# Performance work log

Hardware: AMD Instinct MI355X
Metric: run time of the kernel (lower is better)

## Reference

```python
import jax, jax.numpy as jnp
import numpy as np

NG = 1024      # graphs
NPG = 128      # nodes per graph (forced by lin1 = Linear(128*hid, 128))
N = NG * NPG   # 131072 nodes
DEG = 16       # avg in-graph degree
E = N * DEG    # 2,097,152 edges
IN, H = 4, 64


def setup_inputs() -> dict:
    key = jax.random.key(0)
    ks = jax.random.split(key, 24)
    x = jax.random.normal(ks[0], (N, IN), jnp.float32)
    # edges constrained within each 128-node graph
    src = jax.random.randint(ks[1], (E,), 0, NPG)
    dst = jax.random.randint(ks[2], (E,), 0, NPG)
    off = jnp.repeat(jnp.arange(NG, dtype=jnp.int32) * NPG, NPG * DEG)
    edge_index = jnp.stack([src.astype(jnp.int32) + off, dst.astype(jnp.int32) + off])
    g = lambda k, shp, fan: jax.random.normal(k, shp, jnp.float32) / np.float32(np.sqrt(fan))
    return {
        "x": x, "edge_index": edge_index,
        # GATv2Conv(4->64)
        "Wl": g(ks[3], (IN, H), IN), "bl": jnp.zeros((H,), jnp.float32),
        "Wr": g(ks[4], (IN, H), IN), "br": jnp.zeros((H,), jnp.float32),
        "att_v2": g(ks[5], (H,), H), "b_v2": jnp.zeros((H,), jnp.float32),
        # GATConv #1 (64->64)
        "Wg1": g(ks[6], (H, H), H), "as1": g(ks[7], (H,), H),
        "ad1": g(ks[8], (H,), H), "bg1": jnp.zeros((H,), jnp.float32),
        # GATConv #2 (64->64)
        "Wg2": g(ks[9], (H, H), H), "as2": g(ks[10], (H,), H),
        "ad2": g(ks[11], (H,), H), "bg2": jnp.zeros((H,), jnp.float32),
        # LayerNorm(64)
        "ln_g": jnp.ones((H,), jnp.float32), "ln_b": jnp.zeros((H,), jnp.float32),
        # heads: Linear(128*64 -> 128), Linear(128 -> 1)
        "W1": g(ks[12], (NPG * H, 128), NPG * H), "b1": jnp.zeros((128,), jnp.float32),
        "W2": g(ks[13], (128, 1), 128), "b2": jnp.zeros((1,), jnp.float32),
    }


def _seg_softmax(logits, seg):
    # stable softmax over edges grouped by destination node
    m = jax.ops.segment_max(logits, seg, num_segments=N)
    ex = jnp.exp(logits - m[seg])
    s = jax.ops.segment_sum(ex, seg, num_segments=N)
    return ex / (s[seg] + 1e-16)


def _gatv2(x, src, dst, Wl, bl, Wr, br, att, bias):
    xl = x @ Wl + bl                       # source transform [N,H]
    xr = x @ Wr + br                       # target transform [N,H]
    e = jax.nn.leaky_relu(xl[src] + xr[dst], 0.2) @ att   # [E]
    a = _seg_softmax(e, dst)
    out = jax.ops.segment_sum(a[:, None] * xl[src], dst, num_segments=N)
    return out + bias


def _gat(x, src, dst, W, a_src, a_dst, bias):
    # GATConv default: add self-loops
    loop = jnp.arange(N, dtype=src.dtype)
    s2 = jnp.concatenate([src, loop]); d2 = jnp.concatenate([dst, loop])
    xw = x @ W                             # [N,H]
    al_s = xw @ a_src; al_d = xw @ a_dst   # per-node attention halves [N]
    e = jax.nn.leaky_relu(al_s[s2] + al_d[d2], 0.2)
    a = _seg_softmax(e, d2)
    out = jax.ops.segment_sum(a[:, None] * xw[s2], d2, num_segments=N)
    return out + bias


def _layernorm(x, g, b, eps=1e-5):
    mu = jnp.mean(x, -1, keepdims=True)
    var = jnp.mean(jnp.square(x - mu), -1, keepdims=True)
    return (x - mu) * jax.lax.rsqrt(var + eps) * g + b


def reference(x, edge_index, Wl, bl, Wr, br, att_v2, b_v2,
              Wg1, as1, ad1, bg1, Wg2, as2, ad2, bg2,
              ln_g, ln_b, W1, b1, W2, b2):
    src, dst = edge_index[0], edge_index[1]
    h = jax.nn.leaky_relu(_gatv2(x, src, dst, Wl, bl, Wr, br, att_v2, b_v2), 0.01)
    h = _layernorm(h, ln_g, ln_b)
    h = jax.nn.relu(_gat(h, src, dst, Wg1, as1, ad1, bg1))
    h = jax.nn.relu(_gat(h, src, dst, Wg2, as2, ad2, bg2))
    # linearize: batch is sorted with exactly NPG nodes per graph -> reshape
    h = h.reshape(NG, NPG * H)
    h = jax.nn.leaky_relu(h @ W1 + b1, 0.01)
    return jax.nn.sigmoid(h @ W2 + b2)     # [NG, 1]
```

## Files before the change

### kernel.cpp

```cpp
#include <hip/hip_runtime.h>
#include <hip/hip_bf16.h>

#define NGRAPH 1024
#define NPG 128
#define NTOT (NGRAPH*NPG)
#define EPG 2048
#define ETOT (NTOT*16)
#define HD 64

typedef unsigned int uint;
typedef unsigned short ushort_t;
typedef __attribute__((ext_vector_type(8))) short s8v;
typedef __attribute__((ext_vector_type(4))) float f32x4;

#define MFMA16 __builtin_amdgcn_mfma_f32_16x16x32_bf16

__device__ __forceinline__ float lrelu(float x, float s){ return fmaxf(x, x*s); }
__device__ __forceinline__ float b2lo(uint u){ return __uint_as_float(u << 16); }
__device__ __forceinline__ float b2hi(uint u){ return __uint_as_float(u & 0xFFFF0000u); }
__device__ __forceinline__ uint pkbf(float a, float b){
  union { __hip_bfloat162 h; uint u; } t;
  t.h = __hip_bfloat162{__float2bfloat16(a), __float2bfloat16(b)};
  return t.u;
}
__device__ __forceinline__ ushort_t bfb(float v){
  __hip_bfloat16 h = __float2bfloat16(v);
  union { __hip_bfloat16 h; ushort_t u; } t; t.h = h; return t.u;
}
union U4S8 { uint4 u; s8v s; };
__device__ __forceinline__ s8v bcs8(uint4 u){ U4S8 t; t.u = u; return t.s; }
__device__ __forceinline__ s8v pk8(uint4 x, uint4 y){
  U4S8 t;
  t.u.x = pkbf(__uint_as_float(x.x), __uint_as_float(x.y));
  t.u.y = pkbf(__uint_as_float(x.z), __uint_as_float(x.w));
  t.u.z = pkbf(__uint_as_float(y.x), __uint_as_float(y.y));
  t.u.w = pkbf(__uint_as_float(y.z), __uint_as_float(y.w));
  return t.s;
}

#define DPP_ADD(v, ctrl) ((v) + __int_as_float(__builtin_amdgcn_update_dpp(0, __float_as_int(v), (ctrl), 0xF, 0xF, false)))

__device__ __forceinline__ int oswz(int r, int p){ return (r<<5) | ((((p>>2) ^ (r & 7))<<2) | (p & 3)); }
__device__ __forceinline__ int obase(int r, int oc){ return (r<<5) | (((oc) ^ (r & 7))<<2); }
__device__ __forceinline__ int t64(int r, int p){ return (r<<6) | ((((p>>2) ^ (r & 15))<<2) | (p & 3)); }
__device__ __forceinline__ int t64b(int r, int q){ return (r<<6) | (((q ^ (r & 15))<<2)); }
__device__ __forceinline__ int fP(int r, int k){ return (r<<7) | (((((k>>2) ^ r) & 31)<<2) | (k & 3)); }
__device__ __forceinline__ int fPb(int r, int q){ return (r<<7) | ((((q ^ r) & 31))<<2); }

#define O_A   0
#define O_B   4096
#define O_P   8192
#define O_E   12288
#define O_ED  14336
#define O_SOF 15360
#define O_SPO 15489
#define O_NMV 15617
#define O_SSE 15745
#define O_ALS 15873
#define O_ALD 16001
#define O_WAS 16132
#define O_WAD 16196
#define SM_SZ 16260

__global__ __launch_bounds__(256) void gnn_fused(
    const float* __restrict__ x, const int* __restrict__ ei,
    const float* __restrict__ Wl, const float* __restrict__ bl,
    const float* __restrict__ Wr, const float* __restrict__ br,
    const float* __restrict__ att, const float* __restrict__ bv2,
    const float* __restrict__ Wg1, const float* __restrict__ as1,
    const float* __restrict__ ad1, const float* __restrict__ bg1,
    const float* __restrict__ Wg2, const float* __restrict__ as2,
    const float* __restrict__ ad2, const float* __restrict__ bg2,
    const float* __restrict__ lng, const float* __restrict__ lnb,
    uint* __restrict__ hout)
{
  __shared__ uint SM[SM_SZ];
  uint*     sXl  = SM + O_A;
  uint*     sXr  = SM + O_B;
  float*    Pf   = (float*)(SM + O_P);
  float*    eva  = (float*)(SM + O_E);
  ushort_t* edsd = (ushort_t*)(SM + O_ED);
  int*      soff = (int*)(SM + O_SOF);
  int*      spos = (int*)(SM + O_SPO);
  float*    nmv  = (float*)(SM + O_NMV);
  float*    sse  = (float*)(SM + O_SSE);
  float*    als  = (float*)(SM + O_ALS);
  float*    ald  = (float*)(SM + O_ALD);
  float*    was  = (float*)(SM + O_WAS);
  float*    wad  = (float*)(SM + O_WAD);
  ushort_t* sH16 = (ushort_t*)(SM + O_A);
  ushort_t* sT16 = (ushort_t*)(SM + O_B);
  ushort_t* wg16 = (ushort_t*)(SM + O_E);

  const int g    = blockIdx.x;
  const int tid  = threadIdx.x;
  const int lane = tid & 63;
  const int wv   = tid >> 6;
  const int lw   = lane & 15;
  const int lq   = lane >> 4;
  const int oc   = lane & 7;
  const int ebase = g * EPG;

  if (tid < NPG) spos[tid] = 0;
  __syncthreads();
  for (int e = tid; e < EPG; e += 256)
    atomicAdd(&spos[ei[ETOT + ebase + e] - g*NPG], 1);
  __syncthreads();
  if (wv == 0) {
    int c0 = spos[lane], c1 = spos[lane + 64];
    #pragma unroll
    for (int o = 1; o < 64; o <<= 1) { int t = __shfl_up(c0, o); if (lane >= o) c0 += t; }
    #pragma unroll
    for (int o = 1; o < 64; o <<= 1) { int t = __shfl_up(c1, o); if (lane >= o) c1 += t; }
    int tot0 = __shfl(c0, 63);
    soff[lane + 1]  = c0;
    soff[lane + 65] = c1 + tot0;
    if (lane == 0) soff[0] = 0;
  }
  __syncthreads();
  if (tid < NPG) spos[tid] = soff[tid];
  __syncthreads();
  for (int e = tid; e < EPG; e += 256) {
    int s = ei[ebase + e] - g*NPG;
    int d = ei[ETOT + ebase + e] - g*NPG;
    int p = atomicAdd(&spos[d], 1);
    edsd[p] = (ushort_t)(s | (d << 8));
  }

  {
    const int pl = lane & 31, hb = lane >> 5;
    const float2 wl0 = *(const float2*)&Wl[0*64 + 2*pl];
    const float2 wl1 = *(const float2*)&Wl[1*64 + 2*pl];
    const float2 wl2 = *(const float2*)&Wl[2*64 + 2*pl];
    const float2 wl3 = *(const float2*)&Wl[3*64 + 2*pl];
    const float2 wr0 = *(const float2*)&Wr[0*64 + 2*pl];
    const float2 wr1 = *(const float2*)&Wr[1*64 + 2*pl];
    const float2 wr2 = *(const float2*)&Wr[2*64 + 2*pl];
    const float2 wr3 = *(const float2*)&Wr[3*64 + 2*pl];
    const float2 blp = *(const float2*)&bl[2*pl];
    const float2 brp = *(const float2*)&br[2*pl];
    const float4* x4 = (const float4*)x + (size_t)g * NPG;
    __syncthreads();
    for (int st = 0; st < 16; st++) {
      int i = st*8 + wv*2 + hb;
      float4 xi = x4[i];
      float l0 = blp.x + xi.x*wl0.x + xi.y*wl1.x + xi.z*wl2.x + xi.w*wl3.x;
      float l1 = blp.y + xi.x*wl0.y + xi.y*wl1.y + xi.z*wl2.y + xi.w*wl3.y;
      float r0 = brp.x + xi.x*wr0.x + xi.y*wr1.x + xi.z*wr2.x + xi.w*wr3.x;
      float r1 = brp.y + xi.x*wr0.y + xi.y*wr1.y + xi.z*wr2.y + xi.w*wr3.y;
      sXl[oswz(i, pl)] = pkbf(l0, l1);
      sXr[oswz(i, pl)] = pkbf(r0, r1);
    }
  }
  __syncthreads();

  {
    const int grp = lane >> 3;
    float4 atA = *(const float4*)&att[oc*8];
    float4 atB = *(const float4*)&att[oc*8 + 4];
    int base = wv * 512;
    for (int stp = 0; stp < 64; stp++) {
      int e  = base + stp*8 + grp;
      int sd = edsd[e];
      int s  = sd & 127, d = sd >> 8;
      uint4 ql = *(uint4*)&sXl[obase(s, oc)];
      uint4 qr = *(uint4*)&sXr[obase(d, oc)];
      float acc, v;
      v = b2lo(ql.x)+b2lo(qr.x); acc  = lrelu(v,0.2f)*atA.x;
      v = b2hi(ql.x)+b2hi(qr.x); acc += lrelu(v,0.2f)*atA.y;
      v = b2lo(ql.y)+b2lo(qr.y); acc += lrelu(v,0.2f)*atA.z;
      v = b2hi(ql.y)+b2hi(qr.y); acc += lrelu(v,0.2f)*atA.w;
      v = b2lo(ql.z)+b2lo(qr.z); acc += lrelu(v,0.2f)*atB.x;
      v = b2hi(ql.z)+b2hi(qr.z); acc += lrelu(v,0.2f)*atB.y;
      v = b2lo(ql.w)+b2lo(qr.w); acc += lrelu(v,0.2f)*atB.z;
      v = b2hi(ql.w)+b2hi(qr.w); acc += lrelu(v,0.2f)*atB.w;
      acc = DPP_ADD(acc, 0x111); acc = DPP_ADD(acc, 0x112); acc = DPP_ADD(acc, 0x114);
      if ((lane & 7) == 7) eva[e] = acc;
    }
  }
  __syncthreads();

  {
    const int g16 = tid >> 4, sl = tid & 15;
    for (int it = 0; it < 8; it++) {
      int d = it*16 + g16;
      int p0 = soff[d], p1 = soff[d+1];
      float m = -1e30f;
      for (int p = p0 + sl; p < p1; p += 16) m = fmaxf(m, eva[p]);
      #pragma unroll
      for (int o = 1; o < 16; o <<= 1) m = fmaxf(m, __shfl_xor(m, o));
      float ssum = 0.f;
      for (int p = p0 + sl; p < p1; p += 16) {
        float ex = __expf(eva[p] - m); ssum += ex; eva[p] = ex;
      }
      #pragma unroll
      for (int o = 1; o < 16; o <<= 1) ssum += __shfl_xor(ssum, o);
      if (sl == 0) nmv[d] = 1.f / (ssum + 1e-16f);
    }
    ushort_t* xl16 = (ushort_t*)(SM + O_A);
    int j = tid & 63, spb = tid >> 6;
    for (int i = 0; i < 16; i++) {
      int sp = spb*16 + i;
      float v0 = __uint_as_float((uint)xl16[oswz(2*sp,   j>>1)*2 + (j&1)] << 16);
      float v1 = __uint_as_float((uint)xl16[oswz(2*sp+1, j>>1)*2 + (j&1)] << 16);
      sXr[t64(j, sp)] = pkbf(v0, v1);
    }
  }
  __syncthreads();

  {
    int n0 = 32*(wv>>1), m0 = 16*(wv&1);
    float bja = bv2[n0 + lw], bjb = bv2[n0 + 16 + lw];
    for (int q = 0; q < 4; q++) {
      #pragma unroll
      for (int i = 0; i < 4; i++) { uint4 z = {0,0,0,0}; *(uint4*)&SM[O_P + (tid + i*256)*4] = z; }
      __syncthreads();
      int p0 = soff[q*32], p1 = soff[q*32 + 32];
      for (int p = p0 + tid; p < p1; p += 256) {
        int sd = edsd[p]; int s = sd & 127, d = sd >> 8;
        atomicAdd(&Pf[fP(d - q*32, s)], eva[p] * nmv[d]);
      }
      __syncthreads();
      f32x4 c0 = {0.f,0.f,0.f,0.f}, c1 = {0.f,0.f,0.f,0.f};
      int row = m0 + lw;
      #pragma unroll
      for (int ks = 0; ks < 4; ks++) {
        int kk = ks*32 + lq*8;
        uint4 f0 = *(uint4*)&Pf[fPb(row, kk>>2)];
        uint4 f1 = *(uint4*)&Pf[fPb(row, (kk>>2)+1)];
        s8v a = pk8(f0, f1);
        s8v b0 = bcs8(*(uint4*)&SM[O_B + t64b(n0 + lw,      kk>>3)]);
        s8v b1 = bcs8(*(uint4*)&SM[O_B + t64b(n0 + 16 + lw, kk>>3)]);
        c0 = MFMA16(a, b0, c0, 0, 0, 0);
        c1 = MFMA16(a, b1, c1, 0, 0, 0);
      }
      int rg0 = q*32 + m0 + lq*4;
      #pragma unroll
      for (int rg = 0; rg < 4; rg++) {
        float v0 = lrelu(c0[rg] + bja, 0.01f);
        float v1 = lrelu(c1[rg] + bjb, 0.01f);
        int jc0 = n0 + lw, jc1 = n0 + 16 + lw;
        sH16[oswz(rg0+rg, jc0>>1)*2 + (jc0&1)] = bfb(v0);
        sH16[oswz(rg0+rg, jc1>>1)*2 + (jc1&1)] = bfb(v1);
      }
      __syncthreads();
    }
  }

  {
    int pl = lane & 31, hb = lane >> 5;
    float2 gv = *(const float2*)&lng[2*pl];
    float2 bv = *(const float2*)&lnb[2*pl];
    for (int it = 0; it < 16; it++) {
      int d = it*8 + wv*2 + hb;
      uint w = SM[O_A + oswz(d, pl)];
      float v0 = b2lo(w), v1 = b2hi(w);
      float s1 = v0 + v1, s2 = v0*v0 + v1*v1;
      #pragma unroll
      for (int o = 1; o < 32; o <<= 1) { s1 += __shfl_xor(s1, o); s2 += __shfl_xor(s2, o); }
      float mu  = s1 * 0.015625f;
      float var = s2 * 0.015625f - mu*mu;
      float rs  = rsqrtf(var + 1e-5f);
      v0 = (v0 - mu)*rs*gv.x + bv.x;
      v1 = (v1 - mu)*rs*gv.y + bv.y;
      SM[O_A + oswz(d, pl)] = pkbf(v0, v1);
    }
  }
  __syncthreads();

  for (int layer = 0; layer < 2; layer++) {
    const float* Wg  = layer ? Wg2 : Wg1;
    const float* avs = layer ? as2 : as1;
    const float* avd = layer ? ad2 : ad1;
    const float* bg  = layer ? bg2 : bg1;

    if (tid < 128) {
      const float* av = (tid < 64) ? avs : avd;
      float* dst = (tid < 64) ? was : wad;
      int k = tid & 63;
      float acc = 0.f;
      #pragma unroll
      for (int jj = 0; jj < 16; jj++) {
        float4 w = *(const float4*)&Wg[k*64 + jj*4];
        float4 a = *(const float4*)&av[jj*4];
        acc += w.x*a.x + w.y*a.y + w.z*a.z + w.w*a.w;
      }
      dst[k] = acc;
    } else {
      int t2 = tid - 128;
      #pragma unroll
      for (int i = 0; i < 8; i++) {
        int idx = t2 + i*128;
        int k = idx >> 4, j4 = (idx & 15)*4;
        float4 w = *(const float4*)&Wg[k*64 + j4];
        wg16[oswz(j4+0, k>>1)*2 + (k&1)] = bfb(w.x);
        wg16[oswz(j4+1, k>>1)*2 + (k&1)] = bfb(w.y);
        wg16[oswz(j4+2, k>>1)*2 + (k&1)] = bfb(w.z);
        wg16[oswz(j4+3, k>>1)*2 + (k&1)] = bfb(w.w);
      }
    }
    __syncthreads();

    {
      int row = 16*wv + lw;
      s8v a0 = bcs8(*(uint4*)&SM[O_E + obase(row, lq)]);
      s8v a1 = bcs8(*(uint4*)&SM[O_E + obase(row, 4+lq)]);
      #pragma unroll
      for (int nt = 0; nt < 8; nt++) {
        int d = nt*16 + lw;
        s8v b0 = bcs8(*(uint4*)&SM[O_A + obase(d, lq)]);
        s8v b1 = bcs8(*(uint4*)&SM[O_A + obase(d, 4+lq)]);
        f32x4 c = {0.f,0.f,0.f,0.f};
        c = MFMA16(a0, b0, c, 0, 0, 0);
        c = MFMA16(a1, b1, c, 0, 0, 0);
        int j0 = 16*wv + lq*4;
        #pragma unroll
        for (int rg = 0; rg < 4; rg++)
          sT16[t64(j0+rg, d>>1)*2 + (d&1)] = bfb(c[rg]);
      }
    }
    __syncthreads();

    {
      float4 ws0 = *(float4*)&was[oc*8], ws1 = *(float4*)&was[oc*8 + 4];
      float4 wd0 = *(float4*)&wad[oc*8], wd1 = *(float4*)&wad[oc*8 + 4];
      for (int ps = 0; ps < 4; ps++) {
        int n = ps*32 + (tid >> 3);
        uint4 q = *(uint4*)&SM[O_A + obase(n, oc)];
        float f0=b2lo(q.x), f1=b2hi(q.x), f2=b2lo(q.y), f3=b2hi(q.y);
        float f4=b2lo(q.z), f5=b2hi(q.z), f6=b2lo(q.w), f7=b2hi(q.w);
        float sa = f0*ws0.x+f1*ws0.y+f2*ws0.z+f3*ws0.w+f4*ws1.x+f5*ws1.y+f6*ws1.z+f7*ws1.w;
        float sd = f0*wd0.x+f1*wd0.y+f2*wd0.z+f3*wd0.w+f4*wd1.x+f5*wd1.y+f6*wd1.z+f7*wd1.w;
        sa = DPP_ADD(sa, 0x111); sa = DPP_ADD(sa, 0x112); sa = DPP_ADD(sa, 0x114);
        sd = DPP_ADD(sd, 0x111); sd = DPP_ADD(sd, 0x112); sd = DPP_ADD(sd, 0x114);
        if ((lane & 7) == 7) { als[n] = sa; ald[n] = sd; }
      }
    }
    __syncthreads();

    #pragma unroll
    for (int i = 0; i < 8; i++) {
      int e = tid + i*256;
      int sd = edsd[e];
      eva[e] = lrelu(als[sd & 127] + ald[sd >> 8], 0.2f);
    }
    __syncthreads();

    {
      const int g16 = tid >> 4, sl = tid & 15;
      for (int it = 0; it < 8; it++) {
        int d = it*16 + g16;
        int p0 = soff[d], p1 = soff[d+1];
        float se = lrelu(als[d] + ald[d], 0.2f);
        float m = se;
        for (int p = p0 + sl; p < p1; p += 16) m = fmaxf(m, eva[p]);
        #pragma unroll
        for (int o = 1; o < 16; o <<= 1) m = fmaxf(m, __shfl_xor(m, o));
        float ex0 = __expf(se - m);
        float ssum = 0.f;
        for (int p = p0 + sl; p < p1; p += 16) {
          float ex = __expf(eva[p] - m); ssum += ex; eva[p] = ex;
        }
        #pragma unroll
        for (int o = 1; o < 16; o <<= 1) ssum += __shfl_xor(ssum, o);
        if (sl == 0) { nmv[d] = 1.f / (ssum + ex0 + 1e-16f); sse[d] = ex0; }
      }
    }
    __syncthreads();

    {
      int n0 = 32*(wv>>1), m0 = 16*(wv&1);
      float bja = bg[n0 + lw], bjb = bg[n0 + 16 + lw];
      for (int q = 0; q < 4; q++) {
        #pragma unroll
        for (int i = 0; i < 4; i++) { uint4 z = {0,0,0,0}; *(uint4*)&SM[O_P + (tid + i*256)*4] = z; }
        __syncthreads();
        int p0 = soff[q*32], p1 = soff[q*32 + 32];
        for (int p = p0 + tid; p < p1; p += 256) {
          int sd = edsd[p]; int s = sd & 127, d = sd >> 8;
          atomicAdd(&Pf[fP(d - q*32, s)], eva[p] * nmv[d]);
        }
        if (tid < 32) { int d = q*32 + tid; atomicAdd(&Pf[fP(tid, d)], sse[d] * nmv[d]); }
        __syncthreads();
        f32x4 c0 = {0.f,0.f,0.f,0.f}, c1 = {0.f,0.f,0.f,0.f};
        int row = m0 + lw;
        #pragma unroll
        for (int ks = 0; ks < 4; ks++) {
          int kk = ks*32 + lq*8;
          uint4 f0 = *(uint4*)&Pf[fPb(row, kk>>2)];
          uint4 f1 = *(uint4*)&Pf[fPb(row, (kk>>2)+1)];
          s8v a = pk8(f0, f1);
          s8v b0 = bcs8(*(uint4*)&SM[O_B + t64b(n0 + lw,      kk>>3)]);
          s8v b1 = bcs8(*(uint4*)&SM[O_B + t64b(n0 + 16 + lw, kk>>3)]);
          c0 = MFMA16(a, b0, c0, 0, 0, 0);
          c1 = MFMA16(a, b1, c1, 0, 0, 0);
        }
        int rg0 = q*32 + m0 + lq*4;
        #pragma unroll
        for (int rg = 0; rg < 4; rg++) {
          float v0 = fmaxf(c0[rg] + bja, 0.f);
          float v1 = fmaxf(c1[rg] + bjb, 0.f);
          int jc0 = n0 + lw, jc1 = n0 + 16 + lw;
          sH16[oswz(rg0+rg, jc0>>1)*2 + (jc0&1)] = bfb(v0);
          sH16[oswz(rg0+rg, jc1>>1)*2 + (jc1&1)] = bfb(v1);
        }
        __syncthreads();
      }
    }
  }

  {
    uint* hg = hout + (size_t)g * 4096;
    #pragma unroll
    for (int i = 0; i < 16; i++) {
      int idx = tid + i*256;
      hg[idx] = SM[O_A + oswz(idx >> 5, idx & 31)];
    }
  }
}

__global__ __launch_bounds__(256) void w1_transpose(const float* __restrict__ W1,
                                                    uint* __restrict__ w1t)
{
  __shared__ float sw[64*130];
  const int tid = threadIdx.x;
  const int k0 = blockIdx.x * 64;
  #pragma unroll
  for (int i = 0; i < 8; i++) {
    int idx = tid + i*256;
    int r = idx >> 5, c4 = (idx & 31)*4;
    *(float4*)&sw[r*130 + c4] = *(const float4*)&W1[(size_t)(k0+r)*128 + c4];
  }
  __syncthreads();
  #pragma unroll
  for (int i = 0; i < 16; i++) {
    int idx = tid + i*256;
    int c = idx >> 5, kp = idx & 31;
    w1t[(size_t)c*4096 + (k0>>1) + kp] = pkbf(sw[(2*kp)*130 + c], sw[(2*kp+1)*130 + c]);
  }
}

__global__ __launch_bounds__(256) void head_gemm(
    const uint* __restrict__ hbuf, const uint* __restrict__ w1t,
    float* __restrict__ partial)
{
  __shared__ uint sAh[2048];
  __shared__ uint sBh[4096];
  const int tid = threadIdx.x, lane = tid & 63, wv = tid >> 6;
  const int lw = lane & 15, lq = lane >> 4;
  const int g0 = blockIdx.x * 64;
  const int ks = blockIdx.y;
  f32x4 acc[8];
  #pragma unroll
  for (int i = 0; i < 8; i++) acc[i] = f32x4{0.f,0.f,0.f,0.f};

  for (int ch = 0; ch < 8; ch++) {
    int pb = ks*256 + ch*32;
    #pragma unroll
    for (int i = 0; i < 2; i++) {
      int idx = tid + i*256; int r = idx >> 3, q4 = idx & 7;
      uint4 v = *(const uint4*)&hbuf[(size_t)(g0+r)*4096 + pb + q4*4];
      *(uint4*)&sAh[(r<<5) | ((q4 ^ (r & 7))<<2)] = v;
    }
    #pragma unroll
    for (int i = 0; i < 4; i++) {
      int idx = tid + i*256; int r = idx >> 3, q4 = idx & 7;
      uint4 v = *(const uint4*)&w1t[(size_t)r*4096 + pb + q4*4];
      *(uint4*)&sBh[(r<<5) | ((q4 ^ (r & 7))<<2)] = v;
    }
    __syncthreads();
    int ra = 16*wv + lw;
    s8v a0 = bcs8(*(uint4*)&sAh[obase(ra, lq)]);
    s8v a1 = bcs8(*(uint4*)&sAh[obase(ra, 4+lq)]);
    #pragma unroll
    for (int nt = 0; nt < 8; nt++) {
      int c = nt*16 + lw;
      s8v b0 = bcs8(*(uint4*)&sBh[obase(c, lq)]);
      s8v b1 = bcs8(*(uint4*)&sBh[obase(c, 4+lq)]);
      acc[nt] = MFMA16(a0, b0, acc[nt], 0, 0, 0);
      acc[nt] = MFMA16(a1, b1, acc[nt], 0, 0, 0);
    }
    __syncthreads();
  }
  float* pp = partial + (size_t)ks*131072;
  #pragma unroll
  for (int nt = 0; nt < 8; nt++) {
    int c = nt*16 + lw;
    int r0 = g0 + 16*wv + lq*4;
    #pragma unroll
    for (int rg = 0; rg < 4; rg++)
      pp[(size_t)(r0+rg)*128 + c] = acc[nt][rg];
  }
}

__global__ __launch_bounds__(64) void head_out(
    const float* __restrict__ partial, const float* __restrict__ b1,
    const float* __restrict__ W2, const float* __restrict__ b2,
    float* __restrict__ out)
{
  const int g = blockIdx.x;
  const int l = threadIdx.x;
  float v0 = b1[l], v1 = b1[64 + l];
  #pragma unroll
  for (int s = 0; s < 16; s++) {
    v0 += partial[(size_t)s*131072 + g*128 + l];
    v1 += partial[(size_t)s*131072 + g*128 + 64 + l];
  }
  float sum = lrelu(v0, 0.01f)*W2[l] + lrelu(v1, 0.01f)*W2[64 + l];
  #pragma unroll
  for (int m = 32; m > 0; m >>= 1) sum += __shfl_xor(sum, m);
  if (l == 0) out[g] = 1.f / (1.f + __expf(-(sum + b2[0])));
}

extern "C" void kernel_launch(void* const* d_in, const int* in_sizes, int n_in,
                              void* d_out, int out_size, void* d_ws, size_t ws_size,
                              hipStream_t stream) {
  const float* x   = (const float*)d_in[0];
  const int*   ei  = (const int*)  d_in[1];
  const float* Wl  = (const float*)d_in[2];
  const float* bl_ = (const float*)d_in[3];
  const float* Wr  = (const float*)d_in[4];
  const float* br_ = (const float*)d_in[5];
  const float* att = (const float*)d_in[6];
  const float* bv2 = (const float*)d_in[7];
  const float* Wg1 = (const float*)d_in[8];
  const float* as1 = (const float*)d_in[9];
  const float* ad1 = (const float*)d_in[10];
  const float* bg1 = (const float*)d_in[11];
  const float* Wg2 = (const float*)d_in[12];
  const float* as2 = (const float*)d_in[13];
  const float* ad2 = (const float*)d_in[14];
  const float* bg2 = (const float*)d_in[15];
  const float* lng = (const float*)d_in[16];
  const float* lnb = (const float*)d_in[17];
  const float* W1  = (const float*)d_in[18];
  const float* b1  = (const float*)d_in[19];
  const float* W2  = (const float*)d_in[20];
  const float* b2  = (const float*)d_in[21];
  float* out = (float*)d_out;

  uint*  hbuf    = (uint*)d_ws;
  float* partial = (float*)((char*)d_ws + (size_t)16*1024*1024);
  uint*  w1t     = (uint*)((char*)d_ws + (size_t)24*1024*1024);

  w1_transpose<<<128, 256, 0, stream>>>(W1, w1t);
  gnn_fused<<<NGRAPH, 256, 0, stream>>>(x, ei, Wl, bl_, Wr, br_, att, bv2,
      Wg1, as1, ad1, bg1, Wg2, as2, ad2, bg2, lng, lnb, hbuf);
  head_gemm<<<dim3(16, 16), 256, 0, stream>>>(hbuf, w1t, partial);
  head_out<<<NGRAPH, 64, 0, stream>>>(partial, b1, W2, b2, out);
}
```

Measured before the change: 287.5 us.

## Shrink shared memory: fp16 edge weights, smaller aggregation tiles, recompute GAT logits

Edge attention values are now stored as fp16 in a half-size buffer, and raw GATv2 logits reuse the P scratch region. The dense aggregation works on 16 destination rows per pass instead of 32, so the P tile is halved. The GAT logit pass is dropped and logits are recomputed inside the softmax loops. Together these cut LDS per block from about 65KB to 53KB, aiming for more resident blocks per CU. The cost is twice as many aggregation passes and barriers, and a small precision loss from fp16 edge weights.

```diff
diff --git a/kernel.cpp b/kernel.cpp
--- a/kernel.cpp
+++ b/kernel.cpp
@@ -50,17 +50,17 @@
 #define O_A   0
 #define O_B   4096
 #define O_P   8192
-#define O_E   12288
-#define O_ED  14336
-#define O_SOF 15360
-#define O_SPO 15489
-#define O_NMV 15617
-#define O_SSE 15745
-#define O_ALS 15873
-#define O_ALD 16001
-#define O_WAS 16132
-#define O_WAD 16196
-#define SM_SZ 16260
+#define O_EV  10240
+#define O_ED  11264
+#define O_SOF 12288
+#define O_SPO 12417
+#define O_NMV 12545
+#define O_SSE 12673
+#define O_ALS 12801
+#define O_ALD 12929
+#define O_WAS 13060
+#define O_WAD 13124
+#define SM_SZ 13188
 
 __global__ __launch_bounds__(256) void gnn_fused(
     const float* __restrict__ x, const int* __restrict__ ei,
@@ -75,22 +75,22 @@
     uint* __restrict__ hout)
 {
   __shared__ uint SM[SM_SZ];
-  uint*     sXl  = SM + O_A;
-  uint*     sXr  = SM + O_B;
-  float*    Pf   = (float*)(SM + O_P);
-  float*    eva  = (float*)(SM + O_E);
-  ushort_t* edsd = (ushort_t*)(SM + O_ED);
-  int*      soff = (int*)(SM + O_SOF);
-  int*      spos = (int*)(SM + O_SPO);
-  float*    nmv  = (float*)(SM + O_NMV);
-  float*    sse  = (float*)(SM + O_SSE);
-  float*    als  = (float*)(SM + O_ALS);
-  float*    ald  = (float*)(SM + O_ALD);
-  float*    was  = (float*)(SM + O_WAS);
-  float*    wad  = (float*)(SM + O_WAD);
-  ushort_t* sH16 = (ushort_t*)(SM + O_A);
-  ushort_t* sT16 = (ushort_t*)(SM + O_B);
-  ushort_t* wg16 = (ushort_t*)(SM + O_E);
+  uint*      sXl  = SM + O_A;
+  uint*      sXr  = SM + O_B;
+  float*     Pf   = (float*)(SM + O_P);
+  _Float16*  evh  = (_Float16*)(SM + O_EV);
+  ushort_t*  edsd = (ushort_t*)(SM + O_ED);
+  int*       soff = (int*)(SM + O_SOF);
+  int*       spos = (int*)(SM + O_SPO);
+  float*     nmv  = (float*)(SM + O_NMV);
+  float*     sse  = (float*)(SM + O_SSE);
+  float*     als  = (float*)(SM + O_ALS);
+  float*     ald  = (float*)(SM + O_ALD);
+  float*     was  = (float*)(SM + O_WAS);
+  float*     wad  = (float*)(SM + O_WAD);
+  ushort_t*  sH16 = (ushort_t*)(SM + O_A);
+  ushort_t*  sT16 = (ushort_t*)(SM + O_B);
+  ushort_t*  wg16 = (ushort_t*)(SM + O_P);
 
   const int g    = blockIdx.x;
   const int tid  = threadIdx.x;
@@ -175,7 +175,7 @@
       v = b2lo(ql.w)+b2lo(qr.w); acc += lrelu(v,0.2f)*atB.z;
       v = b2hi(ql.w)+b2hi(qr.w); acc += lrelu(v,0.2f)*atB.w;
       acc = DPP_ADD(acc, 0x111); acc = DPP_ADD(acc, 0x112); acc = DPP_ADD(acc, 0x114);
-      if ((lane & 7) == 7) eva[e] = acc;
+      if ((lane & 7) == 7) Pf[e] = acc;
     }
   }
   __syncthreads();
@@ -186,12 +186,12 @@
       int d = it*16 + g16;
       int p0 = soff[d], p1 = soff[d+1];
       float m = -1e30f;
-      for (int p = p0 + sl; p < p1; p += 16) m = fmaxf(m, eva[p]);
+      for (int p = p0 + sl; p < p1; p += 16) m = fmaxf(m, Pf[p]);
       #pragma unroll
       for (int o = 1; o < 16; o <<= 1) m = fmaxf(m, __shfl_xor(m, o));
       float ssum = 0.f;
       for (int p = p0 + sl; p < p1; p += 16) {
-        float ex = __expf(eva[p] - m); ssum += ex; eva[p] = ex;
+        float ex = __expf(Pf[p] - m); ssum += ex; evh[p] = (_Float16)ex;
       }
       #pragma unroll
       for (int o = 1; o < 16; o <<= 1) ssum += __shfl_xor(ssum, o);
@@ -209,39 +209,34 @@
   __syncthreads();
 
   {
-    int n0 = 32*(wv>>1), m0 = 16*(wv&1);
-    float bja = bv2[n0 + lw], bjb = bv2[n0 + 16 + lw];
-    for (int q = 0; q < 4; q++) {
-      #pragma unroll
-      for (int i = 0; i < 4; i++) { uint4 z = {0,0,0,0}; *(uint4*)&SM[O_P + (tid + i*256)*4] = z; }
+    int n0 = 16*wv;
+    float bja = bv2[n0 + lw];
+    int jc0 = n0 + lw;
+    for (int q = 0; q < 8; q++) {
+      #pragma unroll
+      for (int i = 0; i < 2; i++) { uint4 z = {0,0,0,0}; *(uint4*)&SM[O_P + (tid + i*256)*4] = z; }
       __syncthreads();
-      int p0 = soff[q*32], p1 = soff[q*32 + 32];
+      int p0 = soff[q*16], p1 = soff[q*16 + 16];
       for (int p = p0 + tid; p < p1; p += 256) {
         int sd = edsd[p]; int s = sd & 127, d = sd >> 8;
-        atomicAdd(&Pf[fP(d - q*32, s)], eva[p] * nmv[d]);
+        atomicAdd(&Pf[fP(d - q*16, s)], (float)evh[p] * nmv[d]);
       }
       __syncthreads();
-      f32x4 c0 = {0.f,0.f,0.f,0.f}, c1 = {0.f,0.f,0.f,0.f};
-      int row = m0 + lw;
+      f32x4 c0 = {0.f,0.f,0.f,0.f};
       #pragma unroll
       for (int ks = 0; ks < 4; ks++) {
         int kk = ks*32 + lq*8;
-        uint4 f0 = *(uint4*)&Pf[fPb(row, kk>>2)];
-        uint4 f1 = *(uint4*)&Pf[fPb(row, (kk>>2)+1)];
+        uint4 f0 = *(uint4*)&Pf[fPb(lw, kk>>2)];
+        uint4 f1 = *(uint4*)&Pf[fPb(lw, (kk>>2)+1)];
         s8v a = pk8(f0, f1);
-        s8v b0 = bcs8(*(uint4*)&SM[O_B + t64b(n0 + lw,      kk>>3)]);
-        s8v b1 = bcs8(*(uint4*)&SM[O_B + t64b(n0 + 16 + lw, kk>>3)]);
+        s8v b0 = bcs8(*(uint4*)&SM[O_B + t64b(n0 + lw, kk>>3)]);
         c0 = MFMA16(a, b0, c0, 0, 0, 0);
-        c1 = MFMA16(a, b1, c1, 0, 0, 0);
-      }
-      int rg0 = q*32 + m0 + lq*4;
+      }
+      int rg0 = q*16 + lq*4;
       #pragma unroll
       for (int rg = 0; rg < 4; rg++) {
         float v0 = lrelu(c0[rg] + bja, 0.01f);
-        float v1 = lrelu(c1[rg] + bjb, 0.01f);
-        int jc0 = n0 + lw, jc1 = n0 + 16 + lw;
         sH16[oswz(rg0+rg, jc0>>1)*2 + (jc0&1)] = bfb(v0);
-        sH16[oswz(rg0+rg, jc1>>1)*2 + (jc1&1)] = bfb(v1);
       }
       __syncthreads();
     }
@@ -303,8 +298,8 @@
 
     {
       int row = 16*wv + lw;
-      s8v a0 = bcs8(*(uint4*)&SM[O_E + obase(row, lq)]);
-      s8v a1 = bcs8(*(uint4*)&SM[O_E + obase(row, 4+lq)]);
+      s8v a0 = bcs8(*(uint4*)&SM[O_P + obase(row, lq)]);
+      s8v a1 = bcs8(*(uint4*)&SM[O_P + obase(row, 4+lq)]);
       #pragma unroll
       for (int nt = 0; nt < 8; nt++) {
         int d = nt*16 + lw;
@@ -326,9 +321,9 @@
       float4 wd0 = *(float4*)&wad[oc*8], wd1 = *(float4*)&wad[oc*8 + 4];
       for (int ps = 0; ps < 4; ps++) {
         int n = ps*32 + (tid >> 3);
-        uint4 q = *(uint4*)&SM[O_A + obase(n, oc)];
-        float f0=b2lo(q.x), f1=b2hi(q.x), f2=b2lo(q.y), f3=b2hi(q.y);
-        float f4=b2lo(q.z), f5=b2hi(q.z), f6=b2lo(q.w), f7=b2hi(q.w);
+        uint4 qv = *(uint4*)&SM[O_A + obase(n, oc)];
+        float f0=b2lo(qv.x), f1=b2hi(qv.x), f2=b2lo(qv.y), f3=b2hi(qv.y);
+        float f4=b2lo(qv.z), f5=b2hi(qv.z), f6=b2lo(qv.w), f7=b2hi(qv.w);
         float sa = f0*ws0.x+f1*ws0.y+f2*ws0.z+f3*ws0.w+f4*ws1.x+f5*ws1.y+f6*ws1.z+f7*ws1.w;
         float sd = f0*wd0.x+f1*wd0.y+f2*wd0.z+f3*wd0.w+f4*wd1.x+f5*wd1.y+f6*wd1.z+f7*wd1.w;
         sa = DPP_ADD(sa, 0x111); sa = DPP_ADD(sa, 0x112); sa = DPP_ADD(sa, 0x114);
@@ -338,28 +333,23 @@
     }
     __syncthreads();
 
-    #pragma unroll
-    for (int i = 0; i < 8; i++) {
-      int e = tid + i*256;
-      int sd = edsd[e];
-      eva[e] = lrelu(als[sd & 127] + ald[sd >> 8], 0.2f);
-    }
-    __syncthreads();
-
     {
       const int g16 = tid >> 4, sl = tid & 15;
       for (int it = 0; it < 8; it++) {
         int d = it*16 + g16;
         int p0 = soff[d], p1 = soff[d+1];
-        float se = lrelu(als[d] + ald[d], 0.2f);
+        float adv = ald[d];
+        float se = lrelu(als[d] + adv, 0.2f);
         float m = se;
-        for (int p = p0 + sl; p < p1; p += 16) m = fmaxf(m, eva[p]);
+        for (int p = p0 + sl; p < p1; p += 16)
+          m = fmaxf(m, lrelu(als[edsd[p] & 127] + adv, 0.2f));
         #pragma unroll
         for (int o = 1; o < 16; o <<= 1) m = fmaxf(m, __shfl_xor(m, o));
         float ex0 = __expf(se - m);
         float ssum = 0.f;
         for (int p = p0 + sl; p < p1; p += 16) {
-          float ex = __expf(eva[p] - m); ssum += ex; eva[p] = ex;
+          float ex = __expf(lrelu(als[edsd[p] & 127] + adv, 0.2f) - m);
+          ssum += ex; evh[p] = (_Float16)ex;
         }
         #pragma unroll
         for (int o = 1; o < 16; o <<= 1) ssum += __shfl_xor(ssum, o);
@@ -369,40 +359,35 @@
     __syncthreads();
 
     {
-      int n0 = 32*(wv>>1), m0 = 16*(wv&1);
-      float bja = bg[n0 + lw], bjb = bg[n0 + 16 + lw];
-      for (int q = 0; q < 4; q++) {
+      int n0 = 16*wv;
+      float bja = bg[n0 + lw];
+      int jc0 = n0 + lw;
+      for (int q = 0; q < 8; q++) {
         #pragma unroll
-        for (int i = 0; i < 4; i++) { uint4 z = {0,0,0,0}; *(uint4*)&SM[O_P + (tid + i*256)*4] = z; }
+        for (int i = 0; i < 2; i++) { uint4 z = {0,0,0,0}; *(uint4*)&SM[O_P + (tid + i*256)*4] = z; }
         __syncthreads();
-        int p0 = soff[q*32], p1 = soff[q*32 + 32];
+        int p0 = soff[q*16], p1 = soff[q*16 + 16];
         for (int p = p0 + tid; p < p1; p += 256) {
           int sd = edsd[p]; int s = sd & 127, d = sd >> 8;
-          atomicAdd(&Pf[fP(d - q*32, s)], eva[p] * nmv[d]);
+          atomicAdd(&Pf[fP(d - q*16, s)], (float)evh[p] * nmv[d]);
         }
-        if (tid < 32) { int d = q*32 + tid; atomicAdd(&Pf[fP(tid, d)], sse[d] * nmv[d]); }
+        if (tid < 16) { int d = q*16 + tid; atomicAdd(&Pf[fP(tid, d)], sse[d] * nmv[d]); }
         __syncthreads();
-        f32x4 c0 = {0.f,0.f,0.f,0.f}, c1 = {0.f,0.f,0.f,0.f};
-        int row = m0 + lw;
+        f32x4 c0 = {0.f,0.f,0.f,0.f};
         #pragma unroll
         for (int ks = 0; ks < 4; ks++) {
           int kk = ks*32 + lq*8;
-          uint4 f0 = *(uint4*)&Pf[fPb(row, kk>>2)];
-          uint4 f1 = *(uint4*)&Pf[fPb(row, (kk>>2)+1)];
+          uint4 f0 = *(uint4*)&Pf[fPb(lw, kk>>2)];
+          uint4 f1 = *(uint4*)&Pf[fPb(lw, (kk>>2)+1)];
           s8v a = pk8(f0, f1);
-          s8v b0 = bcs8(*(uint4*)&SM[O_B + t64b(n0 + lw,      kk>>3)]);
-          s8v b1 = bcs8(*(uint4*)&SM[O_B + t64b(n0 + 16 + lw, kk>>3)]);
+          s8v b0 = bcs8(*(uint4*)&SM[O_B + t64b(n0 + lw, kk>>3)]);
           c0 = MFMA16(a, b0, c0, 0, 0, 0);
-          c1 = MFMA16(a, b1, c1, 0, 0, 0);
         }
-        int rg0 = q*32 + m0 + lq*4;
+        int rg0 = q*16 + lq*4;
         #pragma unroll
         for (int rg = 0; rg < 4; rg++) {
           float v0 = fmaxf(c0[rg] + bja, 0.f);
-          float v1 = fmaxf(c1[rg] + bjb, 0.f);
-          int jc0 = n0 + lw, jc1 = n0 + 16 + lw;
           sH16[oswz(rg0+rg, jc0>>1)*2 + (jc0&1)] = bfb(v0);
-          sH16[oswz(rg0+rg, jc1>>1)*2 + (jc1&1)] = bfb(v1);
         }
         __syncthreads();
       }
```

After: 305.6 us. +6.3%, slower.
